# Kernel optimization log

Hardware: AMD Instinct MI355X
Metric: run time of the kernel (lower is better)

The kernel has to match this reference:

```python
import jax, jax.numpy as jnp
import numpy as np

N = 50000          # nodes
E = 800000         # edges (before self-loops)
F_IN = 256         # feature_dim
HEADS = 3
OUT = 128          # per-head channels
HO = HEADS * OUT   # 384
NUM_GRAPHS = 64
NUM_CLASSES = 2
SLOPE = 0.2        # PyG GATConv default negative_slope


def setup_inputs() -> dict:
    key = jax.random.key(0)
    ks = jax.random.split(key, 8)
    x = jax.random.normal(ks[0], (N, F_IN), dtype=jnp.float32)
    edge_index = jax.random.randint(ks[1], (2, E), 0, N)
    batch = jnp.sort(jax.random.randint(ks[2], (N,), 0, NUM_GRAPHS))
    # GATConv params (glorot-ish scales)
    W = jax.random.normal(ks[3], (F_IN, HO), dtype=jnp.float32) * (1.0 / np.sqrt(F_IN))
    att_src = jax.random.normal(ks[4], (HEADS, OUT), dtype=jnp.float32) * 0.1
    att_dst = jax.random.normal(ks[5], (HEADS, OUT), dtype=jnp.float32) * 0.1
    bias = jnp.zeros((HO,), dtype=jnp.float32)
    fc_w = jax.random.normal(ks[6], (HO, NUM_CLASSES), dtype=jnp.float32) * 0.05
    fc_b = jnp.zeros((NUM_CLASSES,), dtype=jnp.float32)
    return {"x": x, "edge_index": edge_index, "batch": batch, "W": W,
            "att_src": att_src, "att_dst": att_dst, "bias": bias,
            "fc_w": fc_w, "fc_b": fc_b}


def reference(x, edge_index, batch, W, att_src, att_dst, bias, fc_w, fc_b):
    n = x.shape[0]
    h = (x @ W).reshape(n, HEADS, OUT)                      # [N, H, C]
    # add self-loops (PyG default add_self_loops=True)
    loops = jnp.arange(n)
    src = jnp.concatenate([edge_index[0], loops])           # [E+N]
    dst = jnp.concatenate([edge_index[1], loops])
    # per-node attention logits
    a_src = jnp.einsum('nhc,hc->nh', h, att_src)            # [N, H]
    a_dst = jnp.einsum('nhc,hc->nh', h, att_dst)
    e = jax.nn.leaky_relu(a_src[src] + a_dst[dst], SLOPE)   # [E+N, H]
    # segment softmax over incoming edges of each dst node
    emax = jax.ops.segment_max(e, dst, num_segments=n)
    ex = jnp.exp(e - emax[dst])
    denom = jax.ops.segment_sum(ex, dst, num_segments=n)
    alpha = ex / (denom[dst] + 1e-16)                       # [E+N, H]
    # weighted scatter-add aggregation
    msg = h[src] * alpha[:, :, None]                        # [E+N, H, C]
    out = jax.ops.segment_sum(msg, dst, num_segments=n)     # [N, H, C]
    out = jax.nn.relu(out.reshape(n, HO) + bias)            # [N, 384]
    # global mean pool per graph
    counts = jax.ops.segment_sum(jnp.ones((n,), out.dtype), batch,
                                 num_segments=NUM_GRAPHS)
    pooled = jax.ops.segment_sum(out, batch, num_segments=NUM_GRAPHS)
    pooled = pooled / jnp.maximum(counts, 1.0)[:, None]     # [G, 384]
    return pooled @ fc_w + fc_b                             # [G, num_classes]
```

## Files before the change

kernel.cpp:

```cpp
#include <hip/hip_runtime.h>
#include <hip/hip_bf16.h>
#include <math.h>

#define HEADS 3
#define HO 384
#define NGRAPH 64
#define F_IN 256
#define SLOPE 0.2f

typedef __attribute__((ext_vector_type(8))) short bf8;
typedef __attribute__((ext_vector_type(4))) float f4;

__device__ __forceinline__ unsigned short bfr(float f) {
    unsigned u = __float_as_uint(f);
    u += 0x7fffu + ((u >> 16) & 1u);
    return (unsigned short)(u >> 16);
}
__device__ __forceinline__ float bflo(unsigned u) { return __uint_as_float(u << 16); }
__device__ __forceinline__ float bfhi(unsigned u) { return __uint_as_float(u & 0xffff0000u); }
__device__ __forceinline__ float lrelu(float v) { return (v > 0.f) ? v : SLOPE * v; }

__global__ __launch_bounds__(256) void misc_k(const int* __restrict__ ei,
                                              const float* __restrict__ W,
                                              const int* __restrict__ batch,
                                              int* __restrict__ count,
                                              short* __restrict__ WbT,
                                              int* __restrict__ gstart,
                                              int NBc, int E, int N) {
    int b = blockIdx.x;
    if (b < NBc) {
        int e = b * 256 + threadIdx.x;
        int ET = E + N;
        if (e >= ET) return;
        int d = (e < E) ? ei[E + e] : (e - E);
        atomicAdd(&count[d], 1);
    } else if (b < NBc + 384) {
        int n = b - NBc;
        int k = threadIdx.x;
        WbT[n * 256 + k] = (short)bfr(W[(size_t)k * HO + n]);
    } else {
        int g = threadIdx.x;
        if (g > NGRAPH) return;
        int lo = 0, hi = N;
        while (lo < hi) { int mid = (lo + hi) >> 1; if (batch[mid] < g) lo = mid + 1; else hi = mid; }
        gstart[g] = lo;
    }
}

#define XS_STRIDE 40
__global__ __launch_bounds__(256, 3) void gemm_att(const float* __restrict__ X,
                                                   const short* __restrict__ WbT,
                                                   const float* __restrict__ att_src,
                                                   const float* __restrict__ att_dst,
                                                   unsigned* __restrict__ Hb,
                                                   float* __restrict__ aSrcO,
                                                   float* __restrict__ aDstO, int N) {
    __shared__ short Xs[64 * XS_STRIDE];
    __shared__ short Bs[384 * XS_STRIDE];
    __shared__ float lsS[64][8];
    __shared__ float lsD[64][8];
    int t = threadIdx.x;
    int w = t >> 6, lane = t & 63;
    int quad = lane >> 4, l15 = lane & 15;
    int rbase = blockIdx.x * 64;

    int sr = t >> 2;
    int sko = (t & 3) * 8;
    int xrow = rbase + sr;
    xrow = (xrow < N) ? xrow : (N - 1);

    f4 acc[4][6] = {};

    for (int k0 = 0; k0 < F_IN; k0 += 32) {
        __syncthreads();
        {
            const float4* xr = (const float4*)(X + (size_t)xrow * F_IN + k0 + sko);
            float4 p0 = xr[0], p1 = xr[1];
            bf8 pk;
            pk[0] = (short)bfr(p0.x); pk[1] = (short)bfr(p0.y);
            pk[2] = (short)bfr(p0.z); pk[3] = (short)bfr(p0.w);
            pk[4] = (short)bfr(p1.x); pk[5] = (short)bfr(p1.y);
            pk[6] = (short)bfr(p1.z); pk[7] = (short)bfr(p1.w);
            *(bf8*)(&Xs[sr * XS_STRIDE + sko]) = pk;
        }
#pragma unroll
        for (int i = 0; i < 6; i++) {
            int n = i * 64 + sr;
            bf8 b = *(const bf8*)(WbT + (size_t)n * F_IN + k0 + sko);
            *(bf8*)(&Bs[n * XS_STRIDE + sko]) = b;
        }
        __syncthreads();
        bf8 ar[4], br[6];
#pragma unroll
        for (int at = 0; at < 4; at++)
            ar[at] = *(const bf8*)(&Xs[(at * 16 + l15) * XS_STRIDE + quad * 8]);
#pragma unroll
        for (int nt = 0; nt < 6; nt++)
            br[nt] = *(const bf8*)(&Bs[(w * 96 + nt * 16 + l15) * XS_STRIDE + quad * 8]);
#pragma unroll
        for (int at = 0; at < 4; at++)
#pragma unroll
            for (int nt = 0; nt < 6; nt++)
                acc[at][nt] = __builtin_amdgcn_mfma_f32_16x16x32_bf16(ar[at], br[nt], acc[at][nt], 0, 0, 0);
    }

    const int splits[4] = {6, 2, 4, 0};
    int split = splits[w];
    float asv[6], adv[6];
#pragma unroll
    for (int nt = 0; nt < 6; nt++) {
        int c = w * 96 + nt * 16 + l15;
        asv[nt] = att_src[c];
        adv[nt] = att_dst[c];
    }
#pragma unroll
    for (int at = 0; at < 4; at++) {
#pragma unroll
        for (int r = 0; r < 4; r++) {
            float paS = 0.f, pbS = 0.f, paD = 0.f, pbD = 0.f;
#pragma unroll
            for (int nt = 0; nt < 6; nt++) {
                float v = acc[at][nt][r];
                if (nt < split) { paS += v * asv[nt]; paD += v * adv[nt]; }
                else            { pbS += v * asv[nt]; pbD += v * adv[nt]; }
            }
#pragma unroll
            for (int off = 1; off < 16; off <<= 1) {
                paS += __shfl_xor(paS, off); pbS += __shfl_xor(pbS, off);
                paD += __shfl_xor(paD, off); pbD += __shfl_xor(pbD, off);
            }
            if (l15 == 0) {
                int row = at * 16 + quad * 4 + r;
                lsS[row][w * 2 + 0] = paS; lsS[row][w * 2 + 1] = pbS;
                lsD[row][w * 2 + 0] = paD; lsD[row][w * 2 + 1] = pbD;
            }
        }
    }
#pragma unroll
    for (int at = 0; at < 4; at++) {
#pragma unroll
        for (int nt = 0; nt < 6; nt++) {
#pragma unroll
            for (int r = 0; r < 4; r++) {
                float v = acc[at][nt][r];
                float vp = __shfl_xor(v, 1);
                int node = rbase + at * 16 + quad * 4 + r;
                if (!(lane & 1) && node < N) {
                    unsigned pk = (unsigned)bfr(v) | ((unsigned)bfr(vp) << 16);
                    Hb[(size_t)node * 192 + w * 48 + nt * 8 + (l15 >> 1)] = pk;
                }
            }
        }
    }
    __syncthreads();
    if (t < 64) {
        int node = rbase + t;
        if (node < N) {
            aSrcO[node * 3 + 0] = lsS[t][0] + lsS[t][2];
            aSrcO[node * 3 + 1] = lsS[t][3] + lsS[t][4];
            aSrcO[node * 3 + 2] = lsS[t][5] + lsS[t][7];
            aDstO[node * 3 + 0] = lsD[t][0] + lsD[t][2];
            aDstO[node * 3 + 1] = lsD[t][3] + lsD[t][4];
            aDstO[node * 3 + 2] = lsD[t][5] + lsD[t][7];
        }
    }
}

__global__ __launch_bounds__(256) void scan_a(const int* __restrict__ count,
                                              int* __restrict__ offsets,
                                              int* __restrict__ bsums, int N) {
    __shared__ int tmp[256];
    int t = threadIdx.x;
    int i = blockIdx.x * 256 + t;
    int v = (i < N) ? count[i] : 0;
    tmp[t] = v;
    __syncthreads();
    for (int off = 1; off < 256; off <<= 1) {
        int x = (t >= off) ? tmp[t - off] : 0;
        __syncthreads();
        tmp[t] += x;
        __syncthreads();
    }
    if (i < N) offsets[i] = tmp[t] - v;
    if (t == 255) bsums[blockIdx.x] = tmp[255];
}

__global__ __launch_bounds__(256) void scan_b(int* __restrict__ bsums, int NB) {
    __shared__ int tmp[256];
    int t = threadIdx.x;
    int v = (t < NB) ? bsums[t] : 0;
    tmp[t] = v;
    __syncthreads();
    for (int off = 1; off < 256; off <<= 1) {
        int x = (t >= off) ? tmp[t - off] : 0;
        __syncthreads();
        tmp[t] += x;
        __syncthreads();
    }
    if (t < NB) bsums[t] = tmp[t] - v;
}

__global__ __launch_bounds__(256) void scan_c(int* __restrict__ offsets,
                                              const int* __restrict__ bsums,
                                              int* __restrict__ cursor, int N) {
    int i = blockIdx.x * 256 + threadIdx.x;
    if (i < N) {
        int o = offsets[i] + bsums[blockIdx.x];
        offsets[i] = o;
        cursor[i] = o;
    }
}

__global__ __launch_bounds__(256) void scatter_k(const int* __restrict__ ei,
                                                 int* __restrict__ cursor,
                                                 int* __restrict__ csr_src, int E, int N) {
    int e = blockIdx.x * 256 + threadIdx.x;
    int ET = E + N;
    if (e >= ET) return;
    int s, d;
    if (e < E) { s = ei[e]; d = ei[E + e]; } else { s = e - E; d = s; }
    int pos = atomicAdd(&cursor[d], 1);
    csr_src[pos] = s;
}

__global__ __launch_bounds__(256) void aggregate_k(const unsigned* __restrict__ Hb,
                                                   const int* __restrict__ csr_src,
                                                   const int* __restrict__ offsets,
                                                   const int* __restrict__ count,
                                                   const float* __restrict__ a_src,
                                                   const float* __restrict__ a_dst,
                                                   const float* __restrict__ bias,
                                                   unsigned* __restrict__ outb, int N) {
    int wid = blockIdx.x * 4 + (threadIdx.x >> 6);
    int lane = threadIdx.x & 63;
    if (wid >= N) return;
    int start = offsets[wid], n = count[wid];
    float ad0 = a_dst[wid * 3 + 0], ad1 = a_dst[wid * 3 + 1], ad2 = a_dst[wid * 3 + 2];
    float a0l = 0.f, a0h = 0.f, a1l = 0.f, a1h = 0.f, a2l = 0.f, a2h = 0.f;

    if (n <= 64) {
        int sreg = 0;
        float l0 = -INFINITY, l1 = -INFINITY, l2 = -INFINITY;
        if (lane < n) {
            sreg = csr_src[start + lane];
            l0 = lrelu(a_src[sreg * 3 + 0] + ad0);
            l1 = lrelu(a_src[sreg * 3 + 1] + ad1);
            l2 = lrelu(a_src[sreg * 3 + 2] + ad2);
        }
        float m0 = l0, m1 = l1, m2 = l2;
#pragma unroll
        for (int off = 1; off < 64; off <<= 1) {
            m0 = fmaxf(m0, __shfl_xor(m0, off));
            m1 = fmaxf(m1, __shfl_xor(m1, off));
            m2 = fmaxf(m2, __shfl_xor(m2, off));
        }
        float e0 = (lane < n) ? expf(l0 - m0) : 0.f;
        float e1 = (lane < n) ? expf(l1 - m1) : 0.f;
        float e2 = (lane < n) ? expf(l2 - m2) : 0.f;
        float s0 = e0, s1 = e1, s2 = e2;
#pragma unroll
        for (int off = 1; off < 64; off <<= 1) {
            s0 += __shfl_xor(s0, off);
            s1 += __shfl_xor(s1, off);
            s2 += __shfl_xor(s2, off);
        }
        float w0r = e0 / (s0 + 1e-16f);
        float w1r = e1 / (s1 + 1e-16f);
        float w2r = e2 / (s2 + 1e-16f);
        int j = 0;
        for (; j + 4 <= n; j += 4) {
            int i0 = __shfl(sreg, j), i1 = __shfl(sreg, j + 1);
            int i2 = __shfl(sreg, j + 2), i3 = __shfl(sreg, j + 3);
            const unsigned* h0 = Hb + (size_t)i0 * 192;
            const unsigned* h1 = Hb + (size_t)i1 * 192;
            const unsigned* h2 = Hb + (size_t)i2 * 192;
            const unsigned* h3 = Hb + (size_t)i3 * 192;
            unsigned u00 = h0[lane], u01 = h0[lane + 64], u02 = h0[lane + 128];
            unsigned u10 = h1[lane], u11 = h1[lane + 64], u12 = h1[lane + 128];
            unsigned u20 = h2[lane], u21 = h2[lane + 64], u22 = h2[lane + 128];
            unsigned u30 = h3[lane], u31 = h3[lane + 64], u32 = h3[lane + 128];
            float w00 = __shfl(w0r, j),     w01 = __shfl(w1r, j),     w02 = __shfl(w2r, j);
            float w10 = __shfl(w0r, j + 1), w11 = __shfl(w1r, j + 1), w12 = __shfl(w2r, j + 1);
            float w20 = __shfl(w0r, j + 2), w21 = __shfl(w1r, j + 2), w22 = __shfl(w2r, j + 2);
            float w30 = __shfl(w0r, j + 3), w31 = __shfl(w1r, j + 3), w32 = __shfl(w2r, j + 3);
            a0l += w00 * bflo(u00) + w10 * bflo(u10) + w20 * bflo(u20) + w30 * bflo(u30);
            a0h += w00 * bfhi(u00) + w10 * bfhi(u10) + w20 * bfhi(u20) + w30 * bfhi(u30);
            a1l += w01 * bflo(u01) + w11 * bflo(u11) + w21 * bflo(u21) + w31 * bflo(u31);
            a1h += w01 * bfhi(u01) + w11 * bfhi(u11) + w21 * bfhi(u21) + w31 * bfhi(u31);
            a2l += w02 * bflo(u02) + w12 * bflo(u12) + w22 * bflo(u22) + w32 * bflo(u32);
            a2h += w02 * bfhi(u02) + w12 * bfhi(u12) + w22 * bfhi(u22) + w32 * bfhi(u32);
        }
        for (; j < n; j++) {
            int si = __shfl(sreg, j);
            const unsigned* h = Hb + (size_t)si * 192;
            unsigned u0 = h[lane], u1 = h[lane + 64], u2 = h[lane + 128];
            float w0 = __shfl(w0r, j), w1 = __shfl(w1r, j), w2 = __shfl(w2r, j);
            a0l += w0 * bflo(u0); a0h += w0 * bfhi(u0);
            a1l += w1 * bflo(u1); a1h += w1 * bfhi(u1);
            a2l += w2 * bflo(u2); a2h += w2 * bfhi(u2);
        }
    } else {
        float m0 = -INFINITY, m1 = -INFINITY, m2 = -INFINITY;
        for (int j = lane; j < n; j += 64) {
            int s = csr_src[start + j];
            m0 = fmaxf(m0, lrelu(a_src[s * 3 + 0] + ad0));
            m1 = fmaxf(m1, lrelu(a_src[s * 3 + 1] + ad1));
            m2 = fmaxf(m2, lrelu(a_src[s * 3 + 2] + ad2));
        }
#pragma unroll
        for (int off = 1; off < 64; off <<= 1) {
            m0 = fmaxf(m0, __shfl_xor(m0, off));
            m1 = fmaxf(m1, __shfl_xor(m1, off));
            m2 = fmaxf(m2, __shfl_xor(m2, off));
        }
        float s0 = 0.f, s1 = 0.f, s2 = 0.f;
        for (int j = lane; j < n; j += 64) {
            int s = csr_src[start + j];
            s0 += expf(lrelu(a_src[s * 3 + 0] + ad0) - m0);
            s1 += expf(lrelu(a_src[s * 3 + 1] + ad1) - m1);
            s2 += expf(lrelu(a_src[s * 3 + 2] + ad2) - m2);
        }
#pragma unroll
        for (int off = 1; off < 64; off <<= 1) {
            s0 += __shfl_xor(s0, off);
            s1 += __shfl_xor(s1, off);
            s2 += __shfl_xor(s2, off);
        }
        float i0 = 1.f / (s0 + 1e-16f), i1 = 1.f / (s1 + 1e-16f), i2 = 1.f / (s2 + 1e-16f);
        for (int j = 0; j < n; j++) {
            int s = csr_src[start + j];
            float w0 = expf(lrelu(a_src[s * 3 + 0] + ad0) - m0) * i0;
            float w1 = expf(lrelu(a_src[s * 3 + 1] + ad1) - m1) * i1;
            float w2 = expf(lrelu(a_src[s * 3 + 2] + ad2) - m2) * i2;
            const unsigned* h = Hb + (size_t)s * 192;
            unsigned u0 = h[lane], u1 = h[lane + 64], u2 = h[lane + 128];
            a0l += w0 * bflo(u0); a0h += w0 * bfhi(u0);
            a1l += w1 * bflo(u1); a1h += w1 * bfhi(u1);
            a2l += w2 * bflo(u2); a2h += w2 * bfhi(u2);
        }
    }

    unsigned* orow = outb + (size_t)wid * 192;
    int c0 = 2 * lane;
    float b0 = bias[c0], b1 = bias[c0 + 1];
    float b2 = bias[128 + c0], b3 = bias[128 + c0 + 1];
    float b4 = bias[256 + c0], b5 = bias[256 + c0 + 1];
    float v, x0, x1;
    unsigned pk;
    v = a0l + b0; x0 = (v > 0.f) ? v : 0.f;
    v = a0h + b1; x1 = (v > 0.f) ? v : 0.f;
    pk = (unsigned)bfr(x0) | ((unsigned)bfr(x1) << 16);
    orow[lane] = pk;
    v = a1l + b2; x0 = (v > 0.f) ? v : 0.f;
    v = a1h + b3; x1 = (v > 0.f) ? v : 0.f;
    pk = (unsigned)bfr(x0) | ((unsigned)bfr(x1) << 16);
    orow[64 + lane] = pk;
    v = a2l + b4; x0 = (v > 0.f) ? v : 0.f;
    v = a2h + b5; x1 = (v > 0.f) ? v : 0.f;
    pk = (unsigned)bfr(x0) | ((unsigned)bfr(x1) << 16);
    orow[128 + lane] = pk;
}

__global__ __launch_bounds__(192) void pool_k(const unsigned* __restrict__ outb,
                                              const int* __restrict__ gstart,
                                              float* __restrict__ pooled) {
    int g = blockIdx.x;
    int chunk = blockIdx.y;
    int t = threadIdx.x;
    int lo = gstart[g], hi = gstart[g + 1];
    float al = 0.f, ah = 0.f;
    for (int r = lo + chunk; r < hi; r += 8) {
        unsigned u = outb[(size_t)r * 192 + t];
        al += bflo(u);
        ah += bfhi(u);
    }
    atomicAdd(&pooled[g * HO + 2 * t], al);
    atomicAdd(&pooled[g * HO + 2 * t + 1], ah);
}

__global__ __launch_bounds__(64) void fc_k(const float* __restrict__ pooled,
                                           const int* __restrict__ gstart,
                                           const float* __restrict__ fc_w,
                                           const float* __restrict__ fc_b,
                                           float* __restrict__ out) {
    int g = blockIdx.x;
    int lane = threadIdx.x;
    float a0 = 0.f, a1 = 0.f;
#pragma unroll
    for (int k = 0; k < 6; k++) {
        int c = lane + 64 * k;
        float pv = pooled[g * HO + c];
        a0 += pv * fc_w[c * 2 + 0];
        a1 += pv * fc_w[c * 2 + 1];
    }
#pragma unroll
    for (int off = 32; off > 0; off >>= 1) {
        a0 += __shfl_down(a0, off);
        a1 += __shfl_down(a1, off);
    }
    if (lane == 0) {
        float cnt = fmaxf((float)(gstart[g + 1] - gstart[g]), 1.0f);
        out[g * 2 + 0] = a0 / cnt + fc_b[0];
        out[g * 2 + 1] = a1 / cnt + fc_b[1];
    }
}

extern "C" void kernel_launch(void* const* d_in, const int* in_sizes, int n_in,
                              void* d_out, int out_size, void* d_ws, size_t ws_size,
                              hipStream_t stream) {
    const float* x       = (const float*)d_in[0];
    const int*   ei      = (const int*)d_in[1];
    const int*   batch   = (const int*)d_in[2];
    const float* W       = (const float*)d_in[3];
    const float* att_src = (const float*)d_in[4];
    const float* att_dst = (const float*)d_in[5];
    const float* bias    = (const float*)d_in[6];
    const float* fc_w    = (const float*)d_in[7];
    const float* fc_b    = (const float*)d_in[8];
    float* out = (float*)d_out;

    const int N = in_sizes[2];
    const int E = in_sizes[1] / 2;
    const int ET = E + N;

    char* p = (char*)d_ws;
    auto alloc = [&](size_t bytes) -> char* {
        char* r = p;
        p += (bytes + 255) & ~(size_t)255;
        return r;
    };
    short*    wbt    = (short*)alloc((size_t)HO * F_IN * 2);
    unsigned* hb     = (unsigned*)alloc((size_t)N * 192 * 4);
    unsigned* outb   = (unsigned*)alloc((size_t)N * 192 * 4);
    float*    a_src  = (float*)alloc((size_t)N * 3 * 4);
    float*    a_dst  = (float*)alloc((size_t)N * 3 * 4);
    char*     zstart = p;
    int*      count  = (int*)alloc((size_t)N * 4);
    float*    pooled = (float*)alloc((size_t)NGRAPH * HO * 4);
    size_t    zbytes = (size_t)(p - zstart);
    int*      offsets = (int*)alloc((size_t)N * 4);
    int*      cursor  = (int*)alloc((size_t)N * 4);
    int*      bsums   = (int*)alloc(4096);
    int*      gstart  = (int*)alloc(1024);
    int*      csr_src = (int*)alloc((size_t)ET * 4);

    hipMemsetAsync(zstart, 0, zbytes, stream);

    int NBc = (ET + 255) / 256;
    misc_k<<<NBc + 384 + 1, 256, 0, stream>>>(ei, W, batch, count, wbt, gstart,
                                              NBc, E, N);
    gemm_att<<<(N + 63) / 64, 256, 0, stream>>>(x, wbt, att_src, att_dst,
                                                hb, a_src, a_dst, N);
    int NB = (N + 255) / 256;
    scan_a<<<NB, 256, 0, stream>>>(count, offsets, bsums, N);
    scan_b<<<1, 256, 0, stream>>>(bsums, NB);
    scan_c<<<NB, 256, 0, stream>>>(offsets, bsums, cursor, N);
    scatter_k<<<(ET + 255) / 256, 256, 0, stream>>>(ei, cursor, csr_src, E, N);
    aggregate_k<<<(N + 3) / 4, 256, 0, stream>>>(hb, csr_src, offsets, count,
                                                 a_src, a_dst, bias, outb, N);
    dim3 pg(NGRAPH, 8);
    pool_k<<<pg, 192, 0, stream>>>(outb, gstart, pooled);
    fc_k<<<NGRAPH, 64, 0, stream>>>(pooled, gstart, fc_w, fc_b, out);

    (void)n_in; (void)out_size; (void)ws_size;
}
```

Baseline: 364.2 us.

## Reuse count-pass atomic ranks for CSR scatter, prefetch X in GEMM, widen gather

The count pass now stores each edge's atomicAdd return value as a rank, so the scatter kernel computes its position as offsets[d]+rank[e] with no second round of atomics and no cursor array. The GEMM prefetches the next X slice into registers before the MFMA loop, overlapping global loads with compute. The aggregation loop issues 8 neighbour row loads per iteration instead of 4 to raise memory-level parallelism. The trade-offs are an extra E+N int array written and read, and higher register pressure in aggregate_k and gemm_att.

```diff
diff --git a/kernel.cpp b/kernel.cpp
--- a/kernel.cpp
+++ b/kernel.cpp
@@ -24,6 +24,7 @@
                                               const float* __restrict__ W,
                                               const int* __restrict__ batch,
                                               int* __restrict__ count,
+                                              int* __restrict__ rank,
                                               short* __restrict__ WbT,
                                               int* __restrict__ gstart,
                                               int NBc, int E, int N) {
@@ -33,7 +34,7 @@
         int ET = E + N;
         if (e >= ET) return;
         int d = (e < E) ? ei[E + e] : (e - E);
-        atomicAdd(&count[d], 1);
+        rank[e] = atomicAdd(&count[d], 1);
     } else if (b < NBc + 384) {
         int n = b - NBc;
         int k = threadIdx.x;
@@ -68,14 +69,16 @@
     int sko = (t & 3) * 8;
     int xrow = rbase + sr;
     xrow = (xrow < N) ? xrow : (N - 1);
+    const float* xrp = X + (size_t)xrow * F_IN;
 
     f4 acc[4][6] = {};
 
+    float4 p0 = *(const float4*)(xrp + sko);
+    float4 p1 = *(const float4*)(xrp + sko + 4);
+
     for (int k0 = 0; k0 < F_IN; k0 += 32) {
         __syncthreads();
         {
-            const float4* xr = (const float4*)(X + (size_t)xrow * F_IN + k0 + sko);
-            float4 p0 = xr[0], p1 = xr[1];
             bf8 pk;
             pk[0] = (short)bfr(p0.x); pk[1] = (short)bfr(p0.y);
             pk[2] = (short)bfr(p0.z); pk[3] = (short)bfr(p0.w);
@@ -90,6 +93,10 @@
             *(bf8*)(&Bs[n * XS_STRIDE + sko]) = b;
         }
         __syncthreads();
+        if (k0 + 32 < F_IN) {
+            p0 = *(const float4*)(xrp + k0 + 32 + sko);
+            p1 = *(const float4*)(xrp + k0 + 32 + sko + 4);
+        }
         bf8 ar[4], br[6];
 #pragma unroll
         for (int at = 0; at < 4; at++)
@@ -201,26 +208,21 @@
 }
 
 __global__ __launch_bounds__(256) void scan_c(int* __restrict__ offsets,
-                                              const int* __restrict__ bsums,
-                                              int* __restrict__ cursor, int N) {
+                                              const int* __restrict__ bsums, int N) {
     int i = blockIdx.x * 256 + threadIdx.x;
-    if (i < N) {
-        int o = offsets[i] + bsums[blockIdx.x];
-        offsets[i] = o;
-        cursor[i] = o;
-    }
+    if (i < N) offsets[i] += bsums[blockIdx.x];
 }
 
 __global__ __launch_bounds__(256) void scatter_k(const int* __restrict__ ei,
-                                                 int* __restrict__ cursor,
+                                                 const int* __restrict__ rank,
+                                                 const int* __restrict__ offsets,
                                                  int* __restrict__ csr_src, int E, int N) {
     int e = blockIdx.x * 256 + threadIdx.x;
     int ET = E + N;
     if (e >= ET) return;
     int s, d;
     if (e < E) { s = ei[e]; d = ei[E + e]; } else { s = e - E; d = s; }
-    int pos = atomicAdd(&cursor[d], 1);
-    csr_src[pos] = s;
+    csr_src[offsets[d] + rank[e]] = s;
 }
 
 __global__ __launch_bounds__(256) void aggregate_k(const unsigned* __restrict__ Hb,
@@ -268,27 +270,25 @@
         float w1r = e1 / (s1 + 1e-16f);
         float w2r = e2 / (s2 + 1e-16f);
         int j = 0;
-        for (; j + 4 <= n; j += 4) {
-            int i0 = __shfl(sreg, j), i1 = __shfl(sreg, j + 1);
-            int i2 = __shfl(sreg, j + 2), i3 = __shfl(sreg, j + 3);
-            const unsigned* h0 = Hb + (size_t)i0 * 192;
-            const unsigned* h1 = Hb + (size_t)i1 * 192;
-            const unsigned* h2 = Hb + (size_t)i2 * 192;
-            const unsigned* h3 = Hb + (size_t)i3 * 192;
-            unsigned u00 = h0[lane], u01 = h0[lane + 64], u02 = h0[lane + 128];
-            unsigned u10 = h1[lane], u11 = h1[lane + 64], u12 = h1[lane + 128];
-            unsigned u20 = h2[lane], u21 = h2[lane + 64], u22 = h2[lane + 128];
-            unsigned u30 = h3[lane], u31 = h3[lane + 64], u32 = h3[lane + 128];
-            float w00 = __shfl(w0r, j),     w01 = __shfl(w1r, j),     w02 = __shfl(w2r, j);
-            float w10 = __shfl(w0r, j + 1), w11 = __shfl(w1r, j + 1), w12 = __shfl(w2r, j + 1);
-            float w20 = __shfl(w0r, j + 2), w21 = __shfl(w1r, j + 2), w22 = __shfl(w2r, j + 2);
-            float w30 = __shfl(w0r, j + 3), w31 = __shfl(w1r, j + 3), w32 = __shfl(w2r, j + 3);
-            a0l += w00 * bflo(u00) + w10 * bflo(u10) + w20 * bflo(u20) + w30 * bflo(u30);
-            a0h += w00 * bfhi(u00) + w10 * bfhi(u10) + w20 * bfhi(u20) + w30 * bfhi(u30);
-            a1l += w01 * bflo(u01) + w11 * bflo(u11) + w21 * bflo(u21) + w31 * bflo(u31);
-            a1h += w01 * bfhi(u01) + w11 * bfhi(u11) + w21 * bfhi(u21) + w31 * bfhi(u31);
-            a2l += w02 * bflo(u02) + w12 * bflo(u12) + w22 * bflo(u22) + w32 * bflo(u32);
-            a2h += w02 * bfhi(u02) + w12 * bfhi(u12) + w22 * bfhi(u22) + w32 * bfhi(u32);
+        for (; j + 8 <= n; j += 8) {
+            int idx[8];
+#pragma unroll
+            for (int q = 0; q < 8; q++) idx[q] = __shfl(sreg, j + q);
+            unsigned u0[8], u1[8], u2[8];
+#pragma unroll
+            for (int q = 0; q < 8; q++) {
+                const unsigned* h = Hb + (size_t)idx[q] * 192;
+                u0[q] = h[lane]; u1[q] = h[lane + 64]; u2[q] = h[lane + 128];
+            }
+#pragma unroll
+            for (int q = 0; q < 8; q++) {
+                float wq0 = __shfl(w0r, j + q);
+                float wq1 = __shfl(w1r, j + q);
+                float wq2 = __shfl(w2r, j + q);
+                a0l += wq0 * bflo(u0[q]); a0h += wq0 * bfhi(u0[q]);
+                a1l += wq1 * bflo(u1[q]); a1h += wq1 * bfhi(u1[q]);
+                a2l += wq2 * bflo(u2[q]); a2h += wq2 * bfhi(u2[q]);
+            }
         }
         for (; j < n; j++) {
             int si = __shfl(sreg, j);
@@ -439,7 +439,7 @@
     float*    pooled = (float*)alloc((size_t)NGRAPH * HO * 4);
     size_t    zbytes = (size_t)(p - zstart);
     int*      offsets = (int*)alloc((size_t)N * 4);
-    int*      cursor  = (int*)alloc((size_t)N * 4);
+    int*      rank    = (int*)alloc((size_t)ET * 4);
     int*      bsums   = (int*)alloc(4096);
     int*      gstart  = (int*)alloc(1024);
     int*      csr_src = (int*)alloc((size_t)ET * 4);
@@ -447,15 +447,15 @@
     hipMemsetAsync(zstart, 0, zbytes, stream);
 
     int NBc = (ET + 255) / 256;
-    misc_k<<<NBc + 384 + 1, 256, 0, stream>>>(ei, W, batch, count, wbt, gstart,
+    misc_k<<<NBc + 384 + 1, 256, 0, stream>>>(ei, W, batch, count, rank, wbt, gstart,
                                               NBc, E, N);
     gemm_att<<<(N + 63) / 64, 256, 0, stream>>>(x, wbt, att_src, att_dst,
                                                 hb, a_src, a_dst, N);
     int NB = (N + 255) / 256;
     scan_a<<<NB, 256, 0, stream>>>(count, offsets, bsums, N);
     scan_b<<<1, 256, 0, stream>>>(bsums, NB);
-    scan_c<<<NB, 256, 0, stream>>>(offsets, bsums, cursor, N);
-    scatter_k<<<(ET + 255) / 256, 256, 0, stream>>>(ei, cursor, csr_src, E, N);
+    scan_c<<<NB, 256, 0, stream>>>(offsets, bsums, N);
+    scatter_k<<<(ET + 255) / 256, 256, 0, stream>>>(ei, rank, offsets, csr_src, E, N);
     aggregate_k<<<(N + 3) / 4, 256, 0, stream>>>(hb, csr_src, offsets, count,
                                                  a_src, a_dst, bias, outb, N);
     dim3 pg(NGRAPH, 8);
```

New measurement: 329.7 us (median of 3 runs). 9.5% less time.
